# Kernel tuning notes

Measured on AMD Instinct MI355X. Metric: run time of the kernel, lower is better.

The kernel has to match this reference:

```python
import jax, jax.numpy as jnp
import numpy as np

NUM_HEADS = 12
HEAD_DIM = 64  # hidden 768 / 12


def setup_inputs() -> dict:
    key = jax.random.key(0)
    k1, k2, k3, k4 = jax.random.split(key, 4)
    B, S, H = 8, 1024, 768
    scale = 1.0 / np.sqrt(H)
    hidden_states = jax.random.normal(k1, (B, S, H), dtype=jnp.float32)
    Wq = jax.random.normal(k2, (H, H), dtype=jnp.float32) * scale
    Wk = jax.random.normal(k3, (H, H), dtype=jnp.float32) * scale
    Wv = jax.random.normal(k4, (H, H), dtype=jnp.float32) * scale
    return {"hidden_states": hidden_states, "Wq": Wq, "Wk": Wk, "Wv": Wv}


def reference(hidden_states, Wq, Wk, Wv):
    B, S, H = hidden_states.shape
    nh, hd = NUM_HEADS, HEAD_DIM
    # Linear projections, no bias. torch Linear: x @ W.T with W of shape [out, in];
    # here weights are stored [out, in] == [H, H].
    def proj(W):
        y = jnp.einsum('bsh,oh->bso', hidden_states, W)
        return y.reshape(B, S, nh, hd).transpose(0, 2, 1, 3)  # [B, nh, S, hd]
    q = proj(Wq)
    k = proj(Wk)
    v = proj(Wv)
    scale = 1.0 / np.sqrt(hd).astype(np.float32)
    scores = jnp.einsum('bhqd,bhkd->bhqk', q, k) * scale  # [B, nh, S, S]
    probs = jax.nn.softmax(scores, axis=-1)
    ctx = jnp.einsum('bhqk,bhkd->bhqd', probs, v)  # [B, nh, S, hd]
    ctx = ctx.transpose(0, 2, 1, 3).reshape(B, S, nh * hd)  # [B, S, H]
    return ctx
```

## Files before the change

kernel.cpp:

```cpp
#include <hip/hip_runtime.h>
#include <hip/hip_fp16.h>

typedef _Float16 f16;
typedef _Float16 f16x4 __attribute__((ext_vector_type(4)));
typedef _Float16 f16x8 __attribute__((ext_vector_type(8)));
typedef float f32x4 __attribute__((ext_vector_type(4)));

#define GLB_AS __attribute__((address_space(1)))
#define LDS_AS __attribute__((address_space(3)))

__device__ __forceinline__ void gload_lds16(const f16* g, f16* lds) {
    __builtin_amdgcn_global_load_lds((const GLB_AS uint32_t*)g,
                                     (LDS_AS uint32_t*)lds, 16, 0, 0);
}

__device__ __forceinline__ int swz(int r, int c8) {
    return r * 64 + (((c8) ^ (r & 7)) << 3);
}

__global__ void cvt_all(const float* __restrict__ hs, const float* __restrict__ wq,
                        const float* __restrict__ wk, const float* __restrict__ wv,
                        f16* __restrict__ hs16, f16* __restrict__ w16) {
    int i = blockIdx.x * 256 + threadIdx.x;
    const float4* src;
    f16x4* dst;
    int off;
    if (i < 1572864) {
        src = (const float4*)hs; dst = (f16x4*)hs16; off = i;
    } else {
        int j = i - 1572864;
        int w = j / 147456;
        off = j - w * 147456;
        src = (const float4*)(w == 0 ? wq : (w == 1 ? wk : wv));
        dst = (f16x4*)(w16 + (size_t)w * 589824);
    }
    float4 v = src[off];
    f16x4 h = {(f16)v.x, (f16)v.y, (f16)v.z, (f16)v.w};
    dst[off] = h;
}

#define QSCALE 0.18033688011112043f

__global__ __launch_bounds__(256, 4) void qkv_gemm(
        const f16* __restrict__ A, const f16* __restrict__ W,
        f16* __restrict__ Qh, f16* __restrict__ Kh, f16* __restrict__ Vth) {
    __shared__ f16 As[128 * 64];
    __shared__ f16 Bs[128 * 64];
    const int m0 = blockIdx.x * 128;
    const int n0 = blockIdx.y * 128;
    const int tid = threadIdx.x;
    const int wave = tid >> 6, lane = tid & 63;
    const int wm = wave & 1, wn = wave >> 1;
    const int quad = lane >> 4, l16 = lane & 15;
    const int srow = lane >> 3;
    const int scol = (((lane & 7) ^ srow) << 3);

    f32x4 acc[4][4] = {};

    const f16* Abase = A + (size_t)m0 * 768;
    const f16* Wbase = W + (size_t)n0 * 768;

    for (int kt = 0; kt < 12; ++kt) {
        const int k0 = kt * 64;
        __syncthreads();
#pragma unroll
        for (int j = 0; j < 4; ++j) {
            int inst = wave * 4 + j;
            int row = inst * 8 + srow;
            gload_lds16(Abase + (size_t)row * 768 + k0 + scol, &As[inst * 512]);
            gload_lds16(Wbase + (size_t)row * 768 + k0 + scol, &Bs[inst * 512]);
        }
        __syncthreads();
#pragma unroll
        for (int kk = 0; kk < 2; ++kk) {
            f16x8 af[4], bf[4];
#pragma unroll
            for (int mi = 0; mi < 4; ++mi) {
                int r = wm * 64 + mi * 16 + l16;
                af[mi] = *(const f16x8*)&As[swz(r, kk * 4 + quad)];
            }
#pragma unroll
            for (int ni = 0; ni < 4; ++ni) {
                int r = wn * 64 + ni * 16 + l16;
                bf[ni] = *(const f16x8*)&Bs[swz(r, kk * 4 + quad)];
            }
#pragma unroll
            for (int mi = 0; mi < 4; ++mi)
#pragma unroll
                for (int ni = 0; ni < 4; ++ni)
                    acc[mi][ni] = __builtin_amdgcn_mfma_f32_16x16x32_f16(
                        af[mi], bf[ni], acc[mi][ni], 0, 0, 0);
        }
    }

    const int seg = n0 / 768;
    const int obase = n0 - seg * 768;
    const float scale = (seg == 0) ? QSCALE : 1.0f;
#pragma unroll
    for (int mi = 0; mi < 4; ++mi) {
#pragma unroll
        for (int ni = 0; ni < 4; ++ni) {
            int o = obase + wn * 64 + ni * 16 + l16;
            int h = o >> 6, d = o & 63;
            if (seg == 2) {
                int gm0 = m0 + wm * 64 + mi * 16 + quad * 4;
                int b = gm0 >> 10, s = gm0 & 1023;
                size_t bh = (size_t)(b * 12 + h);
                f16x4 v4 = {(f16)acc[mi][ni][0], (f16)acc[mi][ni][1],
                            (f16)acc[mi][ni][2], (f16)acc[mi][ni][3]};
                *(f16x4*)&Vth[(bh << 16) + ((size_t)d << 10) + s] = v4;
            } else {
                f16* dst = (seg == 0) ? Qh : Kh;
#pragma unroll
                for (int r = 0; r < 4; ++r) {
                    int gm = m0 + wm * 64 + mi * 16 + quad * 4 + r;
                    int b = gm >> 10, s = gm & 1023;
                    size_t bh = (size_t)(b * 12 + h);
                    dst[((bh << 10 | s) << 6) + d] = (f16)(acc[mi][ni][r] * scale);
                }
            }
        }
    }
}

__global__ __launch_bounds__(256, 4) void attn(
        const f16* __restrict__ Qh, const f16* __restrict__ Kh,
        const f16* __restrict__ Vth, float* __restrict__ out) {
    __shared__ __align__(16) char smem[40960];
    f16* Qs  = (f16*)smem;
    f16* Ks  = (f16*)(smem + 8192);
    f16* Vts = (f16*)(smem + 24576);
    float* rbuf  = (float*)smem;
    float* dbuf  = (float*)(smem + 256);
    float* dump0 = (float*)(smem + 8192);
    float* dump1 = (float*)(smem + 24576);

    const int bh = blockIdx.x;
    const int q0 = blockIdx.y * 64;
    const int b = bh / 12, hh = bh % 12;
    const int tid = threadIdx.x, wave = tid >> 6, lane = tid & 63;
    const int ks = wave & 1, qh = wave >> 1;
    const int quad = lane >> 4, l16 = lane & 15;
    const int srow = lane >> 3;
    const int scol = (((lane & 7) ^ srow) << 3);

    const f16* qbase = Qh + ((size_t)bh * 1024 + q0) * 64;
    const f16* kbase = Kh + (size_t)bh * 1024 * 64;
    const f16* vtbase = Vth + (size_t)bh * 64 * 1024;

#pragma unroll
    for (int j = 0; j < 2; ++j) {
        int inst = wave * 2 + j;
        int row = inst * 8 + srow;
        gload_lds16(qbase + row * 64 + scol, &Qs[inst * 512]);
        gload_lds16(kbase + (size_t)row * 64 + scol, &Ks[inst * 512]);
        gload_lds16(vtbase + (size_t)row * 1024 + scol, &Vts[inst * 512]);
    }
    __syncthreads();

    f16x8 qf[2][2];
#pragma unroll
    for (int t = 0; t < 2; ++t)
#pragma unroll
        for (int kk = 0; kk < 2; ++kk)
            qf[t][kk] = *(const f16x8*)&Qs[swz(qh * 32 + t * 16 + l16, kk * 4 + quad)];

    f32x4 o_acc[2][4] = {};
    float rs[2] = {0.f, 0.f};

    for (int kb = 0; kb < 16; ++kb) {
        const int cur = kb & 1;
        if (kb < 15) {
            const int nk0 = (kb + 1) * 64;
#pragma unroll
            for (int j = 0; j < 2; ++j) {
                int inst = wave * 2 + j;
                int row = inst * 8 + srow;
                gload_lds16(kbase + (size_t)(nk0 + row) * 64 + scol,
                            &Ks[(cur ^ 1) * 4096 + inst * 512]);
                gload_lds16(vtbase + (size_t)row * 1024 + nk0 + scol,
                            &Vts[(cur ^ 1) * 4096 + inst * 512]);
            }
        }

        f16x8 af[2][2];
#pragma unroll
        for (int kh = 0; kh < 2; ++kh) {
            af[kh][0] = *(const f16x8*)&Ks[cur * 4096 + swz(ks * 32 + kh * 16 + l16, quad)];
            af[kh][1] = *(const f16x8*)&Ks[cur * 4096 + swz(ks * 32 + kh * 16 + l16, 4 + quad)];
        }
        f16x4 vf[4][2];
#pragma unroll
        for (int ct = 0; ct < 4; ++ct) {
            int r = ct * 16 + l16;
#pragma unroll
            for (int kh = 0; kh < 2; ++kh) {
                int c8 = ks * 4 + kh * 2 + (quad >> 1);
                vf[ct][kh] = *(const f16x4*)&Vts[cur * 4096 + r * 64 +
                                                 ((c8 ^ (r & 7)) << 3) + (quad & 1) * 4];
            }
        }

#pragma unroll
        for (int t = 0; t < 2; ++t)
#pragma unroll
            for (int kh = 0; kh < 2; ++kh) {
                f32x4 st = {};
                st = __builtin_amdgcn_mfma_f32_16x16x32_f16(af[kh][0], qf[t][0], st, 0, 0, 0);
                st = __builtin_amdgcn_mfma_f32_16x16x32_f16(af[kh][1], qf[t][1], st, 0, 0, 0);
                float e0 = __builtin_amdgcn_exp2f(st[0]);
                float e1 = __builtin_amdgcn_exp2f(st[1]);
                float e2 = __builtin_amdgcn_exp2f(st[2]);
                float e3 = __builtin_amdgcn_exp2f(st[3]);
                rs[t] += (e0 + e1) + (e2 + e3);
                f16x4 pv = {(f16)e0, (f16)e1, (f16)e2, (f16)e3};
#pragma unroll
                for (int ct = 0; ct < 4; ++ct)
                    o_acc[t][ct] = __builtin_amdgcn_mfma_f32_16x16x16f16(
                        pv, vf[ct][kh], o_acc[t][ct], 0, 0, 0);
            }

        if (kb < 15) __syncthreads();
    }

    float rt[2];
#pragma unroll
    for (int t = 0; t < 2; ++t) {
        float v = rs[t];
        v += __shfl_xor(v, 16, 64);
        v += __shfl_xor(v, 32, 64);
        rt[t] = v;
    }

    if (ks == 1) {
        float* dp = qh ? dump1 : dump0;
#pragma unroll
        for (int t = 0; t < 2; ++t)
#pragma unroll
            for (int ct = 0; ct < 4; ++ct)
                *(f32x4*)&dp[(t * 4 + ct) * 256 + lane * 4] = o_acc[t][ct];
        if (quad == 0) {
            rbuf[qh * 32 + l16] = rt[0];
            rbuf[qh * 32 + 16 + l16] = rt[1];
        }
    }
    __syncthreads();
    if (ks == 0) {
        const float* dp = qh ? dump1 : dump0;
#pragma unroll
        for (int t = 0; t < 2; ++t)
#pragma unroll
            for (int ct = 0; ct < 4; ++ct)
                o_acc[t][ct] += *(const f32x4*)&dp[(t * 4 + ct) * 256 + lane * 4];
#pragma unroll
        for (int t = 0; t < 2; ++t) {
            float tot = rt[t] + rbuf[qh * 32 + t * 16 + l16];
            if (quad == 0) dbuf[qh * 32 + t * 16 + l16] = 1.0f / tot;
        }
#pragma unroll
        for (int t = 0; t < 2; ++t) {
            float di[4];
#pragma unroll
            for (int r = 0; r < 4; ++r)
                di[r] = dbuf[qh * 32 + t * 16 + quad * 4 + r];
#pragma unroll
            for (int ct = 0; ct < 4; ++ct)
#pragma unroll
                for (int r = 0; r < 4; ++r) {
                    int s = q0 + qh * 32 + t * 16 + quad * 4 + r;
                    out[((size_t)b * 1024 + s) * 768 + hh * 64 + ct * 16 + l16] =
                        o_acc[t][ct][r] * di[r];
                }
        }
    }
}

extern "C" void kernel_launch(void* const* d_in, const int* in_sizes, int n_in,
                              void* d_out, int out_size, void* d_ws, size_t ws_size,
                              hipStream_t stream) {
    const float* hs = (const float*)d_in[0];
    const float* Wq = (const float*)d_in[1];
    const float* Wk = (const float*)d_in[2];
    const float* Wv = (const float*)d_in[3];
    float* out = (float*)d_out;

    char* ws = (char*)d_ws;
    f16* hs16 = (f16*)ws;
    f16* w16  = (f16*)(ws + 12582912);
    f16* Qh   = (f16*)(ws + 16121856);
    f16* Kh   = (f16*)(ws + 28704768);
    f16* Vth  = (f16*)(ws + 41287680);

    cvt_all<<<7872, 256, 0, stream>>>(hs, Wq, Wk, Wv, hs16, w16);
    qkv_gemm<<<dim3(64, 18), 256, 0, stream>>>(hs16, w16, Qh, Kh, Vth);
    attn<<<dim3(96, 16), 256, 0, stream>>>(Qh, Kh, Vth, out);
    (void)in_sizes; (void)n_in; (void)out_size; (void)ws_size;
}
```

Measured before the change: 158.4 us.

## Give each wave full key range over 32 query rows, doubling query tile

Before, each block handled 64 queries and split the key dimension across wave pairs, merging partial outputs through shared memory at the end. Now each block handles 128 queries and each wave owns 32 query rows over all keys. This removes the cross-wave reduction and its extra barrier, and each K/V tile loaded into shared memory now serves twice as many queries. The cost is more registers per wave for the score tiles, a lower occupancy target, a larger shared-memory footprint, and half as many blocks (768 instead of 1536).

```diff
diff --git a/kernel.cpp b/kernel.cpp
--- a/kernel.cpp
+++ b/kernel.cpp
@@ -123,23 +123,18 @@
     }
 }
 
-__global__ __launch_bounds__(256, 4) void attn(
+__global__ __launch_bounds__(256, 3) void attn(
         const f16* __restrict__ Qh, const f16* __restrict__ Kh,
         const f16* __restrict__ Vth, float* __restrict__ out) {
-    __shared__ __align__(16) char smem[40960];
+    __shared__ __align__(16) char smem[49152];
     f16* Qs  = (f16*)smem;
-    f16* Ks  = (f16*)(smem + 8192);
-    f16* Vts = (f16*)(smem + 24576);
-    float* rbuf  = (float*)smem;
-    float* dbuf  = (float*)(smem + 256);
-    float* dump0 = (float*)(smem + 8192);
-    float* dump1 = (float*)(smem + 24576);
+    f16* Ks  = (f16*)(smem + 16384);
+    f16* Vts = (f16*)(smem + 32768);
 
     const int bh = blockIdx.x;
-    const int q0 = blockIdx.y * 64;
+    const int q0 = blockIdx.y * 128;
     const int b = bh / 12, hh = bh % 12;
     const int tid = threadIdx.x, wave = tid >> 6, lane = tid & 63;
-    const int ks = wave & 1, qh = wave >> 1;
     const int quad = lane >> 4, l16 = lane & 15;
     const int srow = lane >> 3;
     const int scol = (((lane & 7) ^ srow) << 3);
@@ -149,10 +144,15 @@
     const f16* vtbase = Vth + (size_t)bh * 64 * 1024;
 
 #pragma unroll
+    for (int j = 0; j < 4; ++j) {
+        int inst = wave * 4 + j;
+        int row = inst * 8 + srow;
+        gload_lds16(qbase + row * 64 + scol, &Qs[inst * 512]);
+    }
+#pragma unroll
     for (int j = 0; j < 2; ++j) {
         int inst = wave * 2 + j;
         int row = inst * 8 + srow;
-        gload_lds16(qbase + row * 64 + scol, &Qs[inst * 512]);
         gload_lds16(kbase + (size_t)row * 64 + scol, &Ks[inst * 512]);
         gload_lds16(vtbase + (size_t)row * 1024 + scol, &Vts[inst * 512]);
     }
@@ -163,7 +163,7 @@
     for (int t = 0; t < 2; ++t)
 #pragma unroll
         for (int kk = 0; kk < 2; ++kk)
-            qf[t][kk] = *(const f16x8*)&Qs[swz(qh * 32 + t * 16 + l16, kk * 4 + quad)];
+            qf[t][kk] = *(const f16x8*)&Qs[swz(wave * 32 + t * 16 + l16, kk * 4 + quad)];
 
     f32x4 o_acc[2][4] = {};
     float rs[2] = {0.f, 0.f};
@@ -183,95 +183,69 @@
             }
         }
 
-        f16x8 af[2][2];
-#pragma unroll
-        for (int kh = 0; kh < 2; ++kh) {
-            af[kh][0] = *(const f16x8*)&Ks[cur * 4096 + swz(ks * 32 + kh * 16 + l16, quad)];
-            af[kh][1] = *(const f16x8*)&Ks[cur * 4096 + swz(ks * 32 + kh * 16 + l16, 4 + quad)];
-        }
-        f16x4 vf[4][2];
+        f32x4 st[2][4] = {};
 #pragma unroll
         for (int ct = 0; ct < 4; ++ct) {
-            int r = ct * 16 + l16;
-#pragma unroll
-            for (int kh = 0; kh < 2; ++kh) {
-                int c8 = ks * 4 + kh * 2 + (quad >> 1);
-                vf[ct][kh] = *(const f16x4*)&Vts[cur * 4096 + r * 64 +
-                                                 ((c8 ^ (r & 7)) << 3) + (quad & 1) * 4];
-            }
-        }
-
+            f16x8 a0 = *(const f16x8*)&Ks[cur * 4096 + swz(ct * 16 + l16, quad)];
+            f16x8 a1 = *(const f16x8*)&Ks[cur * 4096 + swz(ct * 16 + l16, 4 + quad)];
+#pragma unroll
+            for (int t = 0; t < 2; ++t) {
+                st[t][ct] = __builtin_amdgcn_mfma_f32_16x16x32_f16(a0, qf[t][0], st[t][ct], 0, 0, 0);
+                st[t][ct] = __builtin_amdgcn_mfma_f32_16x16x32_f16(a1, qf[t][1], st[t][ct], 0, 0, 0);
+            }
+        }
+
+        f16x4 pv[2][4];
 #pragma unroll
         for (int t = 0; t < 2; ++t)
 #pragma unroll
-            for (int kh = 0; kh < 2; ++kh) {
-                f32x4 st = {};
-                st = __builtin_amdgcn_mfma_f32_16x16x32_f16(af[kh][0], qf[t][0], st, 0, 0, 0);
-                st = __builtin_amdgcn_mfma_f32_16x16x32_f16(af[kh][1], qf[t][1], st, 0, 0, 0);
-                float e0 = __builtin_amdgcn_exp2f(st[0]);
-                float e1 = __builtin_amdgcn_exp2f(st[1]);
-                float e2 = __builtin_amdgcn_exp2f(st[2]);
-                float e3 = __builtin_amdgcn_exp2f(st[3]);
+            for (int ct = 0; ct < 4; ++ct) {
+                float e0 = __builtin_amdgcn_exp2f(st[t][ct][0]);
+                float e1 = __builtin_amdgcn_exp2f(st[t][ct][1]);
+                float e2 = __builtin_amdgcn_exp2f(st[t][ct][2]);
+                float e3 = __builtin_amdgcn_exp2f(st[t][ct][3]);
                 rs[t] += (e0 + e1) + (e2 + e3);
-                f16x4 pv = {(f16)e0, (f16)e1, (f16)e2, (f16)e3};
+                pv[t][ct] = f16x4{(f16)e0, (f16)e1, (f16)e2, (f16)e3};
+            }
+
+#pragma unroll
+        for (int kc = 0; kc < 4; ++kc) {
+            f16x4 vf[4];
+#pragma unroll
+            for (int ct = 0; ct < 4; ++ct) {
+                int r = ct * 16 + l16;
+                int c8 = kc * 2 + (quad >> 1);
+                vf[ct] = *(const f16x4*)&Vts[cur * 4096 + r * 64 +
+                                             ((c8 ^ (r & 7)) << 3) + (quad & 1) * 4];
+            }
+#pragma unroll
+            for (int t = 0; t < 2; ++t)
 #pragma unroll
                 for (int ct = 0; ct < 4; ++ct)
                     o_acc[t][ct] = __builtin_amdgcn_mfma_f32_16x16x16f16(
-                        pv, vf[ct][kh], o_acc[t][ct], 0, 0, 0);
-            }
+                        pv[t][kc], vf[ct], o_acc[t][ct], 0, 0, 0);
+        }
 
         if (kb < 15) __syncthreads();
     }
 
-    float rt[2];
 #pragma unroll
     for (int t = 0; t < 2; ++t) {
         float v = rs[t];
         v += __shfl_xor(v, 16, 64);
         v += __shfl_xor(v, 32, 64);
-        rt[t] = v;
-    }
-
-    if (ks == 1) {
-        float* dp = qh ? dump1 : dump0;
-#pragma unroll
-        for (int t = 0; t < 2; ++t)
-#pragma unroll
-            for (int ct = 0; ct < 4; ++ct)
-                *(f32x4*)&dp[(t * 4 + ct) * 256 + lane * 4] = o_acc[t][ct];
-        if (quad == 0) {
-            rbuf[qh * 32 + l16] = rt[0];
-            rbuf[qh * 32 + 16 + l16] = rt[1];
-        }
-    }
-    __syncthreads();
-    if (ks == 0) {
-        const float* dp = qh ? dump1 : dump0;
-#pragma unroll
-        for (int t = 0; t < 2; ++t)
-#pragma unroll
-            for (int ct = 0; ct < 4; ++ct)
-                o_acc[t][ct] += *(const f32x4*)&dp[(t * 4 + ct) * 256 + lane * 4];
-#pragma unroll
-        for (int t = 0; t < 2; ++t) {
-            float tot = rt[t] + rbuf[qh * 32 + t * 16 + l16];
-            if (quad == 0) dbuf[qh * 32 + t * 16 + l16] = 1.0f / tot;
-        }
-#pragma unroll
-        for (int t = 0; t < 2; ++t) {
-            float di[4];
-#pragma unroll
-            for (int r = 0; r < 4; ++r)
-                di[r] = dbuf[qh * 32 + t * 16 + quad * 4 + r];
-#pragma unroll
-            for (int ct = 0; ct < 4; ++ct)
-#pragma unroll
-                for (int r = 0; r < 4; ++r) {
-                    int s = q0 + qh * 32 + t * 16 + quad * 4 + r;
-                    out[((size_t)b * 1024 + s) * 768 + hh * 64 + ct * 16 + l16] =
-                        o_acc[t][ct][r] * di[r];
-                }
-        }
+        float di[4];
+#pragma unroll
+        for (int r = 0; r < 4; ++r)
+            di[r] = 1.0f / __shfl(v, quad * 4 + r, 64);
+#pragma unroll
+        for (int ct = 0; ct < 4; ++ct)
+#pragma unroll
+            for (int r = 0; r < 4; ++r) {
+                int s = q0 + wave * 32 + t * 16 + quad * 4 + r;
+                out[((size_t)b * 1024 + s) * 768 + hh * 64 + ct * 16 + l16] =
+                    o_acc[t][ct][r] * di[r];
+            }
     }
 }
 
@@ -293,6 +267,6 @@
 
     cvt_all<<<7872, 256, 0, stream>>>(hs, Wq, Wk, Wv, hs16, w16);
     qkv_gemm<<<dim3(64, 18), 256, 0, stream>>>(hs16, w16, Qh, Kh, Vth);
-    attn<<<dim3(96, 16), 256, 0, stream>>>(Qh, Kh, Vth, out);
+    attn<<<dim3(96, 8), 256, 0, stream>>>(Qh, Kh, Vth, out);
     (void)in_sizes; (void)n_in; (void)out_size; (void)ws_size;
 }
```

Result: faster. 153.6 us (-3.0%).
